# Performance work log

Hardware: AMD Instinct MI355X
Metric: run time of the kernel (lower is better)

The kernel has to match this reference:

```python
import jax, jax.numpy as jnp
import numpy as np
from jax import lax

WIN = 8
SHIFT = 4
NUM_HEADS = 8
DIM = 256
HIDDEN = 1024  # dim * mlp_ratio
EPS = 1e-5


def _layer_norm(x, g, b):
    mu = jnp.mean(x, axis=-1, keepdims=True)
    var = jnp.var(x, axis=-1, keepdims=True)
    return (x - mu) * lax.rsqrt(var + EPS) * g + b


def _window_partition(x, w):
    # x: [B,H,W,C] -> [B*nW, w*w, C]
    B, H, W, C = x.shape
    x = x.reshape(B, H // w, w, W // w, w, C)
    x = x.transpose(0, 1, 3, 2, 4, 5)
    return x.reshape(-1, w * w, C)


def _window_reverse(win, w, H, W):
    C = win.shape[-1]
    B = win.shape[0] // ((H // w) * (W // w))
    x = win.reshape(B, H // w, W // w, w, w, C)
    x = x.transpose(0, 1, 3, 2, 4, 5)
    return x.reshape(B, H, W, C)


def _rel_pos_index(w):
    coords = np.stack(np.meshgrid(np.arange(w), np.arange(w), indexing='ij'))
    cf = coords.reshape(2, -1)
    rel = cf[:, :, None] - cf[:, None, :]
    rel = rel.transpose(1, 2, 0).astype(np.int64)
    rel[:, :, 0] += w - 1
    rel[:, :, 1] += w - 1
    rel[:, :, 0] *= 2 * w - 1
    return rel.sum(-1)  # [w*w, w*w]


def _shift_mask(H, W, w, s):
    img = np.zeros((1, H, W, 1), dtype=np.float32)
    slices = (slice(0, -w), slice(-w, -s), slice(-s, None))
    cnt = 0
    for hs in slices:
        for ws in slices:
            img[:, hs, ws, :] = cnt
            cnt += 1
    mw = img.reshape(1, H // w, w, W // w, w, 1).transpose(0, 1, 3, 2, 4, 5).reshape(-1, w * w)
    diff = mw[:, None, :] - mw[:, :, None]
    return jnp.asarray(np.where(diff != 0, -100.0, 0.0).astype(np.float32))  # [nW,N,N]


def setup_inputs() -> dict:
    key = jax.random.key(0)
    ks = jax.random.split(key, 10)
    d, hid, h = DIM, HIDDEN, NUM_HEADS
    inp = {
        'x': jax.random.normal(ks[0], (2, 16384, d), dtype=jnp.float32),
        'norm1_g': jnp.ones((d,), jnp.float32),
        'norm1_b': jnp.zeros((d,), jnp.float32),
        'qkv_w': jax.random.normal(ks[1], (d, 3 * d), jnp.float32) * 0.02,
        'qkv_b': jnp.zeros((3 * d,), jnp.float32),
        'rel_bias_table': jax.random.normal(ks[2], ((2 * WIN - 1) ** 2, h), jnp.float32) * 0.02,
        'proj_w': jax.random.normal(ks[3], (d, d), jnp.float32) * 0.02,
        'proj_b': jnp.zeros((d,), jnp.float32),
        'norm2_g': jnp.ones((d,), jnp.float32),
        'norm2_b': jnp.zeros((d,), jnp.float32),
        'lin1_w': jax.random.normal(ks[4], (d, hid), jnp.float32) * 0.02,
        'lin1_b': jnp.zeros((hid,), jnp.float32),
        'dw_w': jax.random.normal(ks[5], (hid, 1, 3, 3), jnp.float32) * 0.1,
        'dw_b': jnp.zeros((hid,), jnp.float32),
        'lin2_w': jax.random.normal(ks[6], (hid, d), jnp.float32) * 0.02,
        'lin2_b': jnp.zeros((d,), jnp.float32),
    }
    return inp


def _forward(x, norm1_g, norm1_b, qkv_w, qkv_b, rel_bias_table, proj_w, proj_b,
             norm2_g, norm2_b, lin1_w, lin1_b, dw_w, dw_b, lin2_w, lin2_b):
    B, L, C = x.shape
    H = W = int(np.sqrt(L))
    h, dh = NUM_HEADS, C // NUM_HEADS
    N = WIN * WIN

    shortcut = x
    y = _layer_norm(x, norm1_g, norm1_b).reshape(B, H, W, C)
    if SHIFT > 0:
        y = jnp.roll(y, shift=(-SHIFT, -SHIFT), axis=(1, 2))
        attn_mask = _shift_mask(H, W, WIN, SHIFT)  # [nW,N,N]
    else:
        attn_mask = None

    xw = _window_partition(y, WIN)  # [B_, N, C]
    B_ = xw.shape[0]

    qkv = (xw @ qkv_w + qkv_b).reshape(B_, N, 3, h, dh).transpose(2, 0, 3, 1, 4)
    q, k, v = qkv[0], qkv[1], qkv[2]  # [B_, h, N, dh]
    q = q * (dh ** -0.5)
    attn = jnp.einsum('bhnd,bhmd->bhnm', q, k)

    rpi = _rel_pos_index(WIN)  # [N,N] numpy
    bias = rel_bias_table[rpi.reshape(-1)].reshape(N, N, h).transpose(2, 0, 1)
    attn = attn + bias[None]

    if attn_mask is not None:
        nW = attn_mask.shape[0]
        attn = attn.reshape(B_ // nW, nW, h, N, N) + attn_mask[None, :, None]
        attn = attn.reshape(B_, h, N, N)

    attn = jax.nn.softmax(attn, axis=-1)
    out = jnp.einsum('bhnm,bhmd->bhnd', attn, v).transpose(0, 2, 1, 3).reshape(B_, N, C)
    out = out @ proj_w + proj_b

    y = _window_reverse(out, WIN, H, W)
    if SHIFT > 0:
        y = jnp.roll(y, shift=(SHIFT, SHIFT), axis=(1, 2))
    x = shortcut + y.reshape(B, L, C)

    # LeFF
    z = _layer_norm(x, norm2_g, norm2_b)
    z = jax.nn.gelu(z @ lin1_w + lin1_b, approximate=False)
    z = z.reshape(B, H, W, HIDDEN).transpose(0, 3, 1, 2)  # NCHW
    z = lax.conv_general_dilated(z, dw_w, (1, 1), 'SAME',
                                 feature_group_count=HIDDEN,
                                 dimension_numbers=('NCHW', 'OIHW', 'NCHW'))
    z = jax.nn.gelu(z + dw_b[None, :, None, None], approximate=False)
    z = z.transpose(0, 2, 3, 1).reshape(B, L, HIDDEN)
    z = z @ lin2_w + lin2_b
    return x + z


def reference(x, norm1_g, norm1_b, qkv_w, qkv_b, rel_bias_table, proj_w, proj_b,
              norm2_g, norm2_b, lin1_w, lin1_b, dw_w, dw_b, lin2_w, lin2_b):
    return _forward(x, norm1_g, norm1_b, qkv_w, qkv_b, rel_bias_table, proj_w, proj_b,
                    norm2_g, norm2_b, lin1_w, lin1_b, dw_w, dw_b, lin2_w, lin2_b)
```

## Files before the change

### kernel.cpp

```cpp
#include <hip/hip_runtime.h>
#include <math.h>

#define BATCH 2
#define HW 128
#define CDIM 256
#define LTOK 16384
#define MTOK 32768
#define HEADS 8
#define DH 32
#define WINSZ 8
#define NWIN 64
#define HID 1024

typedef unsigned int  u32;
typedef unsigned short u16;

typedef __attribute__((ext_vector_type(8))) short bf16x8;
typedef __attribute__((ext_vector_type(4))) float f32x4;

__device__ __forceinline__ float gelu_f(float v) {
    return 0.5f * v * (1.f + erff(v * 0.70710678118654752f));
}

__device__ __forceinline__ u16 f2bf(float f) {
    u32 u = __float_as_uint(f);
    u32 r = (u + 0x7fffu + ((u >> 16) & 1u)) >> 16;
    return (u16)r;
}

__device__ __forceinline__ float4 ld4(const float* p) { return *(const float4*)p; }
__device__ __forceinline__ float4 ld4(const u16* p) {
    uint2 v = *(const uint2*)p;
    float4 r;
    r.x = __uint_as_float((v.x & 0xffffu) << 16);
    r.y = __uint_as_float(v.x & 0xffff0000u);
    r.z = __uint_as_float((v.y & 0xffffu) << 16);
    r.w = __uint_as_float(v.y & 0xffff0000u);
    return r;
}
__device__ __forceinline__ void st4(float* p, float4 v) { *(float4*)p = v; }
__device__ __forceinline__ void st4(u16* p, float4 v) {
    uint2 o;
    o.x = (u32)f2bf(v.x) | ((u32)f2bf(v.y) << 16);
    o.y = (u32)f2bf(v.z) | ((u32)f2bf(v.w) << 16);
    *(uint2*)p = o;
}
__device__ __forceinline__ float lds1(const float* p) { return *p; }
__device__ __forceinline__ float lds1(const u16* p) { return __uint_as_float(((u32)*p) << 16); }
__device__ __forceinline__ void sts1(float* p, float v) { *p = v; }
__device__ __forceinline__ void sts1(u16* p, float v) { *p = f2bf(v); }

__device__ __forceinline__ void ld8bf(const u16* p, float* v) {
    uint4 r = *(const uint4*)p;
    v[0] = __uint_as_float((r.x & 0xffffu) << 16);
    v[1] = __uint_as_float(r.x & 0xffff0000u);
    v[2] = __uint_as_float((r.y & 0xffffu) << 16);
    v[3] = __uint_as_float(r.y & 0xffff0000u);
    v[4] = __uint_as_float((r.z & 0xffffu) << 16);
    v[5] = __uint_as_float(r.z & 0xffff0000u);
    v[6] = __uint_as_float((r.w & 0xffffu) << 16);
    v[7] = __uint_as_float(r.w & 0xffff0000u);
}

__device__ __forceinline__ void glds16(const u16* g, u16* l) {
    __builtin_amdgcn_global_load_lds(
        (const __attribute__((address_space(1))) unsigned int*)g,
        (__attribute__((address_space(3))) unsigned int*)l, 16, 0, 0);
}

__global__ __launch_bounds__(256) void transpose_bf16_kernel(
    const float* __restrict__ in, u16* __restrict__ out, int K, int N)
{
    __shared__ float t[32][33];
    int bn = blockIdx.x * 32, bk = blockIdx.y * 32;
    int tx = threadIdx.x & 31, ty = threadIdx.x >> 5;
    #pragma unroll
    for (int i = 0; i < 32; i += 8)
        t[ty + i][tx] = in[(size_t)(bk + ty + i) * N + bn + tx];
    __syncthreads();
    #pragma unroll
    for (int i = 0; i < 32; i += 8)
        out[(size_t)(bn + ty + i) * K + bk + tx] = f2bf(t[tx][ty + i]);
}

__global__ __launch_bounds__(256) void dwprep_kernel(
    const float* __restrict__ in, float* __restrict__ out)
{
    int idx = blockIdx.x * 256 + threadIdx.x;
    if (idx < 9 * HID) {
        int ch = idx / 9, t = idx - ch * 9;
        out[t * HID + ch] = in[idx];
    }
}

template<typename TI, typename TO>
__global__ __launch_bounds__(256) void ln_kernel(
    const TI* __restrict__ x, const float* __restrict__ g,
    const float* __restrict__ b, TO* __restrict__ y)
{
    int wave = threadIdx.x >> 6;
    int lane = threadIdx.x & 63;
    int row = blockIdx.x * 4 + wave;
    const TI* xr = x + (size_t)row * CDIM;
    float4 v = ld4(&xr[lane * 4]);
    float s  = v.x + v.y + v.z + v.w;
    float s2 = v.x*v.x + v.y*v.y + v.z*v.z + v.w*v.w;
    #pragma unroll
    for (int off = 32; off > 0; off >>= 1) {
        s  += __shfl_xor(s,  off);
        s2 += __shfl_xor(s2, off);
    }
    float mu   = s * (1.f / CDIM);
    float var  = s2 * (1.f / CDIM) - mu * mu;
    float rstd = rsqrtf(var + 1e-5f);
    float4 gv = *(const float4*)&g[lane * 4];
    float4 bv = *(const float4*)&b[lane * 4];
    float4 o;
    o.x = (v.x - mu) * rstd * gv.x + bv.x;
    o.y = (v.y - mu) * rstd * gv.y + bv.y;
    o.z = (v.z - mu) * rstd * gv.z + bv.z;
    o.w = (v.w - mu) * rstd * gv.w + bv.w;
    st4(&y[(size_t)row * CDIM + lane * 4], o);
}

template<int EPI, int K, typename TR, typename TO>
__global__ __launch_bounds__(256) void mgemm_kernel(
    const u16* __restrict__ A, const u16* __restrict__ Bt,
    const float* __restrict__ bias, const TR* __restrict__ res,
    TO* __restrict__ Cc, int N, int gx)
{
    __shared__ u16 As[128 * 64];
    __shared__ u16 Bs[128 * 64];

    int tid  = threadIdx.x;
    int lane = tid & 63;
    int wave = tid >> 6;
    int l15  = lane & 15;
    int hi   = lane >> 4;
    int wr = wave >> 1, wc = wave & 1;

    int nwg = gridDim.x;
    int bid = blockIdx.x;
    int swz = (bid & 7) * (nwg >> 3) + (bid >> 3);
    int bx = swz % gx, by = swz / gx;
    size_t bm = (size_t)by * 128;
    size_t bn = (size_t)bx * 128;

    int srow8 = lane >> 3;
    int ce    = (lane & 7) * 8;

    int ar = wr * 64 + l15;
    int br = wc * 64 + l15;

    f32x4 acc[4][4] = {};

    for (int t = 0; t < K / 64; ++t) {
        int kt = t * 64;
        #pragma unroll
        for (int g = 0; g < 4; ++g) {
            int rowb = wave * 32 + g * 8;
            int row  = rowb + srow8;
            int col  = kt + (ce ^ ((row & 7) << 3));
            glds16(A  + (bm + row) * K + col, As + rowb * 64);
            glds16(Bt + (bn + row) * K + col, Bs + rowb * 64);
        }
        __syncthreads();

        #pragma unroll
        for (int ks = 0; ks < 2; ++ks) {
            int e = ks * 32 + hi * 8;
            bf16x8 af[4], bfv[4];
            #pragma unroll
            for (int m = 0; m < 4; ++m) {
                int row = ar + m * 16;
                af[m] = *(const bf16x8*)&As[row * 64 + (e ^ ((row & 7) << 3))];
            }
            #pragma unroll
            for (int n = 0; n < 4; ++n) {
                int row = br + n * 16;
                bfv[n] = *(const bf16x8*)&Bs[row * 64 + (e ^ ((row & 7) << 3))];
            }
            #pragma unroll
            for (int m = 0; m < 4; ++m)
                #pragma unroll
                for (int n = 0; n < 4; ++n)
                    acc[m][n] = __builtin_amdgcn_mfma_f32_16x16x32_bf16(
                        af[m], bfv[n], acc[m][n], 0, 0, 0);
        }
        __syncthreads();
    }

    int colb = (int)bn + wc * 64 + l15;
    int rowb = (int)bm + wr * 64 + hi * 4;
    #pragma unroll
    for (int n = 0; n < 4; ++n) {
        float bv = bias[colb + n * 16];
        #pragma unroll
        for (int m = 0; m < 4; ++m) {
            #pragma unroll
            for (int r = 0; r < 4; ++r) {
                int row = rowb + m * 16 + r;
                float v = acc[m][n][r] + bv;
                if (EPI == 1) v += lds1(&res[(size_t)row * N + colb + n * 16]);
                if (EPI == 2) v = gelu_f(v);
                sts1(&Cc[(size_t)row * N + colb + n * 16], v);
            }
        }
    }
}

__global__ __launch_bounds__(64) void attn_mfma_kernel(
    const u16* __restrict__ qkv, const float* __restrict__ bias_table,
    u16* __restrict__ out)
{
    __shared__ u16 P[NWIN * NWIN];
    __shared__ int lbl[NWIN];

    int lane = threadIdx.x;
    int l15 = lane & 15;
    int hi  = lane >> 4;
    int widx = blockIdx.x;
    int head = blockIdx.y;
    int b  = widx >> 8;
    int w  = widx & 255;
    int wr = w >> 4, wc = w & 15;

    auto tokof = [&](int n) -> int {
        int si = (wr * WINSZ + (n >> 3) + 4) & 127;
        int sj = (wc * WINSZ + (n & 7) + 4) & 127;
        return b * LTOK + si * HW + sj;
    };

    {
        int i = wr * WINSZ + (lane >> 3);
        int j = wc * WINSZ + (lane & 7);
        int li = (i < 120) ? 0 : (i < 124 ? 1 : 2);
        int lj = (j < 120) ? 0 : (j < 124 ? 1 : 2);
        lbl[lane] = li * 3 + lj;
    }

    bf16x8 qf[4], kf[4];
    #pragma unroll
    for (int m = 0; m < 4; ++m) {
        int t = tokof(m * 16 + l15);
        const u16* base = qkv + (size_t)t * 768 + head * DH + hi * 8;
        qf[m] = *(const bf16x8*)base;
        kf[m] = *(const bf16x8*)(base + 256);
    }

    bf16x8 vf[2][2];
    #pragma unroll
    for (int ks = 0; ks < 2; ++ks) {
        #pragma unroll
        for (int i = 0; i < 8; ++i) {
            int t = tokof(ks * 32 + hi * 8 + i);
            const u16* vb = qkv + (size_t)t * 768 + 512 + head * DH;
            vf[0][ks][i] = (short)vb[l15];
            vf[1][ks][i] = (short)vb[16 + l15];
        }
    }

    f32x4 s[4][4];
    #pragma unroll
    for (int m = 0; m < 4; ++m)
        #pragma unroll
        for (int n = 0; n < 4; ++n) {
            f32x4 z = {0.f, 0.f, 0.f, 0.f};
            s[m][n] = __builtin_amdgcn_mfma_f32_16x16x32_bf16(qf[m], kf[n], z, 0, 0, 0);
        }

    __syncthreads();

    int klbl[4];
    #pragma unroll
    for (int n = 0; n < 4; ++n) klbl[n] = lbl[n * 16 + l15];

    const float SCALE = 0.17677669529663687f;
    float inv[4][4];
    #pragma unroll
    for (int m = 0; m < 4; ++m) {
        #pragma unroll
        for (int r = 0; r < 4; ++r) {
            int q = m * 16 + hi * 4 + r;
            int qlbl = lbl[q];
            int rq = q >> 3, cq = q & 7;
            float v[4];
            #pragma unroll
            for (int n = 0; n < 4; ++n) {
                int kn = n * 16 + l15;
                int idx = (rq - (kn >> 3) + 7) * 15 + (cq - (kn & 7) + 7);
                float bv = bias_table[idx * HEADS + head];
                v[n] = s[m][n][r] * SCALE + bv + ((klbl[n] != qlbl) ? -100.f : 0.f);
            }
            float rmax = fmaxf(fmaxf(v[0], v[1]), fmaxf(v[2], v[3]));
            #pragma unroll
            for (int off = 1; off < 16; off <<= 1)
                rmax = fmaxf(rmax, __shfl_xor(rmax, off));
            float p0 = __expf(v[0] - rmax), p1 = __expf(v[1] - rmax);
            float p2 = __expf(v[2] - rmax), p3 = __expf(v[3] - rmax);
            float ls = p0 + p1 + p2 + p3;
            #pragma unroll
            for (int off = 1; off < 16; off <<= 1)
                ls += __shfl_xor(ls, off);
            inv[m][r] = 1.f / ls;
            int sw = (q & 7) << 3;
            P[q * NWIN + ((0 * 16 + l15) ^ sw)] = f2bf(p0);
            P[q * NWIN + ((1 * 16 + l15) ^ sw)] = f2bf(p1);
            P[q * NWIN + ((2 * 16 + l15) ^ sw)] = f2bf(p2);
            P[q * NWIN + ((3 * 16 + l15) ^ sw)] = f2bf(p3);
        }
    }

    __syncthreads();

    f32x4 o[4][2] = {};
    #pragma unroll
    for (int ks = 0; ks < 2; ++ks) {
        #pragma unroll
        for (int m = 0; m < 4; ++m) {
            int row = m * 16 + l15;
            int colb = (ks * 32 + hi * 8) ^ ((row & 7) << 3);
            bf16x8 pa = *(const bf16x8*)&P[row * NWIN + colb];
            #pragma unroll
            for (int nf = 0; nf < 2; ++nf)
                o[m][nf] = __builtin_amdgcn_mfma_f32_16x16x32_bf16(
                    pa, vf[nf][ks], o[m][nf], 0, 0, 0);
        }
    }

    #pragma unroll
    for (int m = 0; m < 4; ++m) {
        #pragma unroll
        for (int r = 0; r < 4; ++r) {
            int q = m * 16 + hi * 4 + r;
            int t = tokof(q);
            u16* op = out + (size_t)t * CDIM + head * DH + l15;
            float iv = inv[m][r];
            op[0]  = f2bf(o[m][0][r] * iv);
            op[16] = f2bf(o[m][1][r] * iv);
        }
    }
}

__global__ __launch_bounds__(256) void dwconv_kernel(
    const u16* __restrict__ h, const float* __restrict__ wt9,
    const float* __restrict__ bias, u16* __restrict__ out)
{
    int blk = blockIdx.x;
    int b   = blk >> 11;
    int rem = blk & 2047;
    int i   = rem >> 4;
    int jt  = rem & 15;
    int cg  = (threadIdx.x & 127) * 8;
    int j0  = jt * 8 + (threadIdx.x >> 7) * 4;

    float acc[4][8] = {};
    const u16* base = h + (size_t)b * LTOK * HID + cg;

    #pragma unroll
    for (int di = 0; di < 3; ++di) {
        int ii = i + di - 1;
        if (ii < 0 || ii >= HW) continue;
        const u16* rowp = base + (size_t)ii * HW * HID;
        float v[6][8];
        #pragma unroll
        for (int cc = 0; cc < 6; ++cc) {
            int jj = j0 - 1 + cc;
            if (jj >= 0 && jj < HW) {
                ld8bf(&rowp[(size_t)jj * HID], v[cc]);
            } else {
                #pragma unroll
                for (int q = 0; q < 8; ++q) v[cc][q] = 0.f;
            }
        }
        #pragma unroll
        for (int t = 0; t < 3; ++t) {
            const float* wp = &wt9[(di * 3 + t) * HID + cg];
            float4 wa = *(const float4*)wp;
            float4 wb = *(const float4*)(wp + 4);
            float w[8] = {wa.x, wa.y, wa.z, wa.w, wb.x, wb.y, wb.z, wb.w};
            #pragma unroll
            for (int p = 0; p < 4; ++p)
                #pragma unroll
                for (int q = 0; q < 8; ++q)
                    acc[p][q] += v[p + t][q] * w[q];
        }
    }

    float4 ba = *(const float4*)&bias[cg];
    float4 bb = *(const float4*)&bias[cg + 4];
    float bs[8] = {ba.x, ba.y, ba.z, ba.w, bb.x, bb.y, bb.z, bb.w};
    u16* ob = out + ((size_t)b * LTOK + (size_t)i * HW + j0) * HID + cg;
    #pragma unroll
    for (int p = 0; p < 4; ++p) {
        u32 o[4];
        #pragma unroll
        for (int q = 0; q < 4; ++q) {
            u16 lo = f2bf(gelu_f(acc[p][2 * q] + bs[2 * q]));
            u16 hi = f2bf(gelu_f(acc[p][2 * q + 1] + bs[2 * q + 1]));
            o[q] = (u32)lo | ((u32)hi << 16);
        }
        *(uint4*)(ob + (size_t)p * HID) = make_uint4(o[0], o[1], o[2], o[3]);
    }
}

extern "C" void kernel_launch(void* const* d_in, const int* in_sizes, int n_in,
                              void* d_out, int out_size, void* d_ws, size_t ws_size,
                              hipStream_t stream) {
    const float* x      = (const float*)d_in[0];
    const float* n1g    = (const float*)d_in[1];
    const float* n1b    = (const float*)d_in[2];
    const float* qkv_w  = (const float*)d_in[3];
    const float* qkv_b  = (const float*)d_in[4];
    const float* relb   = (const float*)d_in[5];
    const float* proj_w = (const float*)d_in[6];
    const float* proj_b = (const float*)d_in[7];
    const float* n2g    = (const float*)d_in[8];
    const float* n2b    = (const float*)d_in[9];
    const float* lin1_w = (const float*)d_in[10];
    const float* lin1_b = (const float*)d_in[11];
    const float* dw_w   = (const float*)d_in[12];
    const float* dw_b   = (const float*)d_in[13];
    const float* lin2_w = (const float*)d_in[14];
    const float* lin2_b = (const float*)d_in[15];
    float* out = (float*)d_out;

    u16* ws16 = (u16*)d_ws;
    const size_t M8 = (size_t)MTOK * CDIM;
    u16* yn      = ws16;
    u16* qkv     = ws16 + M8;
    u16* attn    = ws16;
    u16* x1      = ws16 + 4 * M8;
    u16* yn2     = ws16;
    u16* hbuf    = ws16 + 5 * M8;
    u16* h2      = ws16;
    u16* qkv_wt  = ws16 + 5 * M8;
    u16* proj_wt = qkv_wt + 768 * 256;
    u16* lin1_wt = ws16 + M8;
    u16* lin2_wt = ws16 + 5 * M8;
    float* wt9   = (float*)d_out;

    transpose_bf16_kernel<<<dim3(768 / 32, 256 / 32), 256, 0, stream>>>(qkv_w, qkv_wt, 256, 768);
    transpose_bf16_kernel<<<dim3(256 / 32, 256 / 32), 256, 0, stream>>>(proj_w, proj_wt, 256, 256);
    ln_kernel<float, u16><<<MTOK / 4, 256, 0, stream>>>(x, n1g, n1b, yn);
    mgemm_kernel<0, CDIM, float, u16><<<(768 / 128) * (MTOK / 128), 256, 0, stream>>>(
        yn, qkv_wt, qkv_b, (const float*)nullptr, qkv, 768, 768 / 128);
    attn_mfma_kernel<<<dim3(512, HEADS), 64, 0, stream>>>(qkv, relb, attn);
    transpose_bf16_kernel<<<dim3(1024 / 32, 256 / 32), 256, 0, stream>>>(lin1_w, lin1_wt, 256, 1024);
    dwprep_kernel<<<36, 256, 0, stream>>>(dw_w, wt9);
    mgemm_kernel<1, CDIM, float, u16><<<(CDIM / 128) * (MTOK / 128), 256, 0, stream>>>(
        attn, proj_wt, proj_b, x, x1, CDIM, CDIM / 128);
    ln_kernel<u16, u16><<<MTOK / 4, 256, 0, stream>>>(x1, n2g, n2b, yn2);
    mgemm_kernel<2, CDIM, float, u16><<<(HID / 128) * (MTOK / 128), 256, 0, stream>>>(
        yn2, lin1_wt, lin1_b, (const float*)nullptr, hbuf, HID, HID / 128);
    dwconv_kernel<<<BATCH * 2048, 256, 0, stream>>>(hbuf, wt9, dw_b, h2);
    transpose_bf16_kernel<<<dim3(256 / 32, 1024 / 32), 256, 0, stream>>>(lin2_w, lin2_wt, 1024, 256);
    mgemm_kernel<1, HID, u16, float><<<(CDIM / 128) * (MTOK / 128), 256, 0, stream>>>(
        h2, lin2_wt, lin2_b, x1, out, CDIM, CDIM / 128);

    (void)in_sizes; (void)n_in; (void)out_size; (void)ws_size;
}
```

Before: 279.5 us.

## Fuse QKV projection GEMM into window attention kernel

```diff
diff --git a/kernel.cpp b/kernel.cpp
--- a/kernel.cpp
+++ b/kernel.cpp
@@ -209,54 +209,127 @@
     }
 }
 
-__global__ __launch_bounds__(64) void attn_mfma_kernel(
-    const u16* __restrict__ qkv, const float* __restrict__ bias_table,
+__global__ __launch_bounds__(512) void fused_qkv_attn_kernel(
+    const u16* __restrict__ yn, const u16* __restrict__ qkv_wt,
+    const float* __restrict__ qkv_b, const float* __restrict__ bias_table,
     u16* __restrict__ out)
 {
-    __shared__ u16 P[NWIN * NWIN];
-    __shared__ int lbl[NWIN];
-
-    int lane = threadIdx.x;
-    int l15 = lane & 15;
-    int hi  = lane >> 4;
-    int widx = blockIdx.x;
-    int head = blockIdx.y;
-    int b  = widx >> 8;
-    int w  = widx & 255;
-    int wr = w >> 4, wc = w & 15;
+    __shared__ u16 lds[8][4096];
+
+    int tid  = threadIdx.x;
+    int lane = tid & 63;
+    int head = tid >> 6;
+    int l15  = lane & 15;
+    int hi   = lane >> 4;
+    int w  = blockIdx.x;
+    int b  = w >> 8;
+    int ww = w & 255;
+    int wr = ww >> 4, wc = ww & 15;
+    u16* L = lds[head];
 
     auto tokof = [&](int n) -> int {
         int si = (wr * WINSZ + (n >> 3) + 4) & 127;
         int sj = (wc * WINSZ + (n & 7) + 4) & 127;
         return b * LTOK + si * HW + sj;
     };
-
-    {
-        int i = wr * WINSZ + (lane >> 3);
-        int j = wc * WINSZ + (lane & 7);
+    auto labelof = [&](int n) -> int {
+        int i = wr * WINSZ + (n >> 3);
+        int j = wc * WINSZ + (n & 7);
         int li = (i < 120) ? 0 : (i < 124 ? 1 : 2);
         int lj = (j < 120) ? 0 : (j < 124 ? 1 : 2);
-        lbl[lane] = li * 3 + lj;
-    }
-
+        return li * 3 + lj;
+    };
+
+    const u16* arow[4];
+    #pragma unroll
+    for (int m = 0; m < 4; ++m)
+        arow[m] = yn + (size_t)tokof(m * 16 + l15) * CDIM + hi * 8;
+
+    f32x4 qa[4][2] = {}, ka[4][2] = {};
+    #pragma unroll
+    for (int kb = 0; kb < 8; ++kb) {
+        bf16x8 a[4];
+        #pragma unroll
+        for (int m = 0; m < 4; ++m)
+            a[m] = *(const bf16x8*)(arow[m] + kb * 32);
+        #pragma unroll
+        for (int nf = 0; nf < 2; ++nf) {
+            const u16* wp = qkv_wt +
+                (size_t)(head * 32 + nf * 16 + l15) * CDIM + kb * 32 + hi * 8;
+            bf16x8 bq = *(const bf16x8*)wp;
+            bf16x8 bk = *(const bf16x8*)(wp + 256 * CDIM);
+            #pragma unroll
+            for (int m = 0; m < 4; ++m) {
+                qa[m][nf] = __builtin_amdgcn_mfma_f32_16x16x32_bf16(a[m], bq, qa[m][nf], 0, 0, 0);
+                ka[m][nf] = __builtin_amdgcn_mfma_f32_16x16x32_bf16(a[m], bk, ka[m][nf], 0, 0, 0);
+            }
+        }
+    }
+    #pragma unroll
+    for (int nf = 0; nf < 2; ++nf) {
+        int d = nf * 16 + l15;
+        float bq = qkv_b[head * 32 + d];
+        float bk = qkv_b[256 + head * 32 + d];
+        int g = nf * 2 + (l15 >> 3);
+        #pragma unroll
+        for (int m = 0; m < 4; ++m)
+            #pragma unroll
+            for (int r = 0; r < 4; ++r) {
+                int tok = m * 16 + hi * 4 + r;
+                int ad = tok * 32 + ((g ^ r ^ hi) << 3) + (d & 7);
+                L[ad]        = f2bf(qa[m][nf][r] + bq);
+                L[2048 + ad] = f2bf(ka[m][nf][r] + bk);
+            }
+    }
     bf16x8 qf[4], kf[4];
-    #pragma unroll
-    for (int m = 0; m < 4; ++m) {
-        int t = tokof(m * 16 + l15);
-        const u16* base = qkv + (size_t)t * 768 + head * DH + hi * 8;
-        qf[m] = *(const bf16x8*)base;
-        kf[m] = *(const bf16x8*)(base + 256);
-    }
-
+    {
+        int sz = (hi ^ (l15 & 3) ^ ((l15 >> 2) & 3)) << 3;
+        #pragma unroll
+        for (int m = 0; m < 4; ++m) {
+            int ra = (m * 16 + l15) * 32 + sz;
+            qf[m] = *(const bf16x8*)&L[ra];
+            kf[m] = *(const bf16x8*)&L[2048 + ra];
+        }
+    }
+
+    f32x4 va[4][2] = {};
+    #pragma unroll
+    for (int kb = 0; kb < 8; ++kb) {
+        bf16x8 a[4];
+        #pragma unroll
+        for (int m = 0; m < 4; ++m)
+            a[m] = *(const bf16x8*)(arow[m] + kb * 32);
+        #pragma unroll
+        for (int nf = 0; nf < 2; ++nf) {
+            const u16* wp = qkv_wt +
+                (size_t)(512 + head * 32 + nf * 16 + l15) * CDIM + kb * 32 + hi * 8;
+            bf16x8 bv = *(const bf16x8*)wp;
+            #pragma unroll
+            for (int m = 0; m < 4; ++m)
+                va[m][nf] = __builtin_amdgcn_mfma_f32_16x16x32_bf16(a[m], bv, va[m][nf], 0, 0, 0);
+        }
+    }
+    #pragma unroll
+    for (int nf = 0; nf < 2; ++nf) {
+        int d = nf * 16 + l15;
+        float bv = qkv_b[512 + head * 32 + d];
+        #pragma unroll
+        for (int m = 0; m < 4; ++m)
+            #pragma unroll
+            for (int r = 0; r < 4; ++r) {
+                int tok = m * 16 + hi * 4 + r;
+                int av = d * 64 + (((tok >> 3) ^ (d & 7)) << 3) + (tok & 7);
+                L[av] = f2bf(va[m][nf][r] + bv);
+            }
+    }
     bf16x8 vf[2][2];
     #pragma unroll
-    for (int ks = 0; ks < 2; ++ks) {
-        #pragma unroll
-        for (int i = 0; i < 8; ++i) {
-            int t = tokof(ks * 32 + hi * 8 + i);
-            const u16* vb = qkv + (size_t)t * 768 + 512 + head * DH;
-            vf[0][ks][i] = (short)vb[l15];
-            vf[1][ks][i] = (short)vb[16 + l15];
+    for (int nf = 0; nf < 2; ++nf) {
+        int d = nf * 16 + l15;
+        #pragma unroll
+        for (int ks = 0; ks < 2; ++ks) {
+            int rv = d * 64 + (((ks * 4 + hi) ^ (d & 7)) << 3);
+            vf[nf][ks] = *(const bf16x8*)&L[rv];
         }
     }
 
@@ -269,11 +342,9 @@
             s[m][n] = __builtin_amdgcn_mfma_f32_16x16x32_bf16(qf[m], kf[n], z, 0, 0, 0);
         }
 
-    __syncthreads();
-
     int klbl[4];
     #pragma unroll
-    for (int n = 0; n < 4; ++n) klbl[n] = lbl[n * 16 + l15];
+    for (int n = 0; n < 4; ++n) klbl[n] = labelof(n * 16 + l15);
 
     const float SCALE = 0.17677669529663687f;
     float inv[4][4];
@@ -282,7 +353,7 @@
         #pragma unroll
         for (int r = 0; r < 4; ++r) {
             int q = m * 16 + hi * 4 + r;
-            int qlbl = lbl[q];
+            int qlbl = labelof(q);
             int rq = q >> 3, cq = q & 7;
             float v[4];
             #pragma unroll
@@ -304,14 +375,12 @@
                 ls += __shfl_xor(ls, off);
             inv[m][r] = 1.f / ls;
             int sw = (q & 7) << 3;
-            P[q * NWIN + ((0 * 16 + l15) ^ sw)] = f2bf(p0);
-            P[q * NWIN + ((1 * 16 + l15) ^ sw)] = f2bf(p1);
-            P[q * NWIN + ((2 * 16 + l15) ^ sw)] = f2bf(p2);
-            P[q * NWIN + ((3 * 16 + l15) ^ sw)] = f2bf(p3);
-        }
-    }
-
-    __syncthreads();
+            L[q * 64 + ((0 * 16 + l15) ^ sw)] = f2bf(p0);
+            L[q * 64 + ((1 * 16 + l15) ^ sw)] = f2bf(p1);
+            L[q * 64 + ((2 * 16 + l15) ^ sw)] = f2bf(p2);
+            L[q * 64 + ((3 * 16 + l15) ^ sw)] = f2bf(p3);
+        }
+    }
 
     f32x4 o[4][2] = {};
     #pragma unroll
@@ -320,7 +389,7 @@
         for (int m = 0; m < 4; ++m) {
             int row = m * 16 + l15;
             int colb = (ks * 32 + hi * 8) ^ ((row & 7) << 3);
-            bf16x8 pa = *(const bf16x8*)&P[row * NWIN + colb];
+            bf16x8 pa = *(const bf16x8*)&L[row * 64 + colb];
             #pragma unroll
             for (int nf = 0; nf < 2; ++nf)
                 o[m][nf] = __builtin_amdgcn_mfma_f32_16x16x32_bf16(
@@ -428,24 +497,21 @@
     u16* ws16 = (u16*)d_ws;
     const size_t M8 = (size_t)MTOK * CDIM;
     u16* yn      = ws16;
-    u16* qkv     = ws16 + M8;
-    u16* attn    = ws16;
+    u16* attn    = ws16 + M8;
     u16* x1      = ws16 + 4 * M8;
     u16* yn2     = ws16;
     u16* hbuf    = ws16 + 5 * M8;
     u16* h2      = ws16;
     u16* qkv_wt  = ws16 + 5 * M8;
     u16* proj_wt = qkv_wt + 768 * 256;
-    u16* lin1_wt = ws16 + M8;
+    u16* lin1_wt = ws16 + 2 * M8;
     u16* lin2_wt = ws16 + 5 * M8;
     float* wt9   = (float*)d_out;
 
     transpose_bf16_kernel<<<dim3(768 / 32, 256 / 32), 256, 0, stream>>>(qkv_w, qkv_wt, 256, 768);
     transpose_bf16_kernel<<<dim3(256 / 32, 256 / 32), 256, 0, stream>>>(proj_w, proj_wt, 256, 256);
     ln_kernel<float, u16><<<MTOK / 4, 256, 0, stream>>>(x, n1g, n1b, yn);
-    mgemm_kernel<0, CDIM, float, u16><<<(768 / 128) * (MTOK / 128), 256, 0, stream>>>(
-        yn, qkv_wt, qkv_b, (const float*)nullptr, qkv, 768, 768 / 128);
-    attn_mfma_kernel<<<dim3(512, HEADS), 64, 0, stream>>>(qkv, relb, attn);
+    fused_qkv_attn_kernel<<<512, 512, 0, stream>>>(yn, qkv_wt, qkv_b, relb, attn);
     transpose_bf16_kernel<<<dim3(1024 / 32, 256 / 32), 256, 0, stream>>>(lin1_w, lin1_wt, 256, 1024);
     dwprep_kernel<<<36, 256, 0, stream>>>(dw_w, wt9);
     mgemm_kernel<1, CDIM, float, u16><<<(CDIM / 128) * (MTOK / 128), 256, 0, stream>>>(
```

After: 276.8 us. No clear change (-1.0%).
